# Kernel optimization log

Hardware: AMD Instinct MI355X
Metric: run time of the kernel (lower is better)

Reference implementation:

```python
import jax, jax.numpy as jnp
import numpy as np

D_SVG, N_TYPE, N_PAR = 256, 10, 12          # deep-svg latent, animation types, animation params
PADDING_VALUE = -1.0
W_SVG, W_TYPE, W_PAR = 10.0, 0.1, 1.0       # weight_deep_svg, weight_type, weight_parameters

# ANIMATION_PARAMETER_INDICES as a dense boolean lookup: type t -> which params it uses
_pm = np.zeros((N_TYPE, N_PAR), dtype=bool)
for _t in range(N_TYPE):
    for _k in (_t % N_PAR, (_t + 1) % N_PAR, (_t + 2) % N_PAR):
        _pm[_t, _k] = True
PARAM_MASK = jnp.asarray(_pm)


def setup_inputs() -> dict:
    B, S = 256, 512
    F = D_SVG + N_TYPE + N_PAR
    key = jax.random.key(0)
    k1, k2, k3, k4, k5 = jax.random.split(key, 5)
    x = jax.random.normal(k1, (B, S, F), dtype=jnp.float32)
    cls = jax.random.randint(k2, (B, S), 0, N_TYPE)
    t_type = jax.nn.one_hot(cls, N_TYPE, dtype=jnp.float32)
    t_svg = jax.random.normal(k3, (B, S, D_SVG), dtype=jnp.float32)
    t_par = jax.random.normal(k4, (B, S, N_PAR), dtype=jnp.float32)
    target = jnp.concatenate([t_svg, t_type, t_par], axis=-1)
    # suffix-contiguous padding (matches the `break` semantics of the torch loop)
    lengths = jax.random.randint(k5, (B,), S // 2, S + 1)
    mask = jnp.arange(S)[None, :] >= lengths[:, None]            # True = padded
    target = jnp.where(mask[..., None], PADDING_VALUE, target)
    return {"input": x, "target": target, "target_padding_mask": mask}


def reference(input, target, target_padding_mask):
    # input[expanded_mask] = -100
    x = jnp.where(target_padding_mask[..., None], -100.0, input)
    in_svg, in_type, in_par = jnp.split(x, [D_SVG, D_SVG + N_TYPE], axis=-1)
    tg_svg, tg_type, tg_par = jnp.split(target, [D_SVG, D_SVG + N_TYPE], axis=-1)

    valid = tg_type[..., 0] != PADDING_VALUE                      # [B,S] non-padded rows
    t_idx = jnp.argmax(tg_type, axis=-1)                          # [B,S] animation type

    # vectorized replacement of the double for-loop: copy target params at the
    # type-dependent ANIMATION_PARAMETER_INDICES into input params
    pmask = PARAM_MASK[t_idx] & valid[..., None]                  # [B,S,N_PAR]
    in_par = jnp.where(pmask, tg_par, in_par)

    # CrossEntropyLoss(ignore_index=-1) over flattened type logits
    logits = in_type.reshape(-1, N_TYPE)
    labels = t_idx.reshape(-1)
    v = valid.reshape(-1).astype(logits.dtype)
    logp = jax.nn.log_softmax(logits, axis=-1)
    nll = -jnp.take_along_axis(logp, labels[:, None], axis=1)[:, 0]
    loss_type = jnp.sum(nll * v) / jnp.maximum(jnp.sum(v), 1.0)

    # plain MSE (mean over ALL elements, padding included, as in the original)
    loss_svg = jnp.mean((in_svg - tg_svg) ** 2)
    loss_par = jnp.mean((in_par - tg_par) ** 2)

    return W_SVG * loss_svg + W_TYPE * loss_type + W_PAR * loss_par
```

## Files before the change

### kernel.cpp

```cpp
#include <hip/hip_runtime.h>
#include <hip/hip_bf16.h>
#include <math.h>

#define D_SVG 256
#define N_TYPE 10
#define N_PAR 12
#define F_TOT (D_SVG + N_TYPE + N_PAR)
#define ROWS_PER_BLOCK 32
#define THREADS 256
#define N4_PER_BLOCK (ROWS_PER_BLOCK * F_TOT / 4)
#define FULL_ITERS (N4_PER_BLOCK / THREADS)
#define TAIL (N4_PER_BLOCK - FULL_ITERS * THREADS)

#define PAD_SVG_BLOCK (9801.0f * D_SVG * ROWS_PER_BLOCK)
#define PAD_PAR_BLOCK (9801.0f * N_PAR * ROWS_PER_BLOCK)


__global__ __launch_bounds__(THREADS) void loss_main(const float* __restrict__ input,
                                                     const float* __restrict__ target,
                                                     float4* __restrict__ part,
                                                     int nrows) {
    __shared__ unsigned smeta[ROWS_PER_BLOCK];
    __shared__ unsigned long long sballot;
    __shared__ float sred[4][4];

    const int tid = threadIdx.x;
    const long row0 = (long)blockIdx.x * ROWS_PER_BLOCK;

    float nll_acc = 0.0f;
    float cnt_acc = 0.0f;

    if (tid < ROWS_PER_BLOCK) {
        unsigned meta = 0u;
        long r = row0 + tid;
        long b2 = (r * F_TOT + D_SVG) >> 1;
        const float2* __restrict__ tg2 = (const float2*)target;
        const float2* __restrict__ in2 = (const float2*)input;
        float2 t01 = tg2[b2];
        if (t01.x != -1.0f) {
            float tg[N_TYPE], l[N_TYPE];
            tg[0] = t01.x; tg[1] = t01.y;
            #pragma unroll
            for (int j = 1; j < 5; ++j) { float2 v = tg2[b2 + j]; tg[2*j] = v.x; tg[2*j+1] = v.y; }
            #pragma unroll
            for (int j = 0; j < 5; ++j) { float2 v = in2[b2 + j]; l[2*j] = v.x; l[2*j+1] = v.y; }
            int ti = 0; float best = tg[0];
            #pragma unroll
            for (int j = 1; j < N_TYPE; ++j) { if (tg[j] > best) { best = tg[j]; ti = j; } }
            float m = l[0];
            #pragma unroll
            for (int j = 1; j < N_TYPE; ++j) m = fmaxf(m, l[j]);
            float s = 0.0f;
            #pragma unroll
            for (int j = 0; j < N_TYPE; ++j) s += __expf(l[j] - m);
            nll_acc = __logf(s) + m - l[ti];
            cnt_acc = 1.0f;
            meta = 0x80000000u | (7u << ti);
        }
        smeta[tid] = meta;
        unsigned long long bal = __ballot(meta != 0u);
        if (tid == 0) sballot = bal;
    }
    __syncthreads();

    if (sballot == 0ull) {
        if (tid == 0) part[blockIdx.x] = make_float4(PAD_SVG_BLOCK, PAD_PAR_BLOCK, 0.0f, 0.0f);
        return;
    }

    float svg_acc = 0.0f, par_acc = 0.0f;
    const float4* __restrict__ in4p = (const float4*)(input + row0 * F_TOT);
    const float4* __restrict__ tg4p = (const float4*)(target + row0 * F_TOT);

    float4 iv[FULL_ITERS], tv[FULL_ITERS];
    #pragma unroll
    for (int u = 0; u < FULL_ITERS; ++u) iv[u] = in4p[tid + u * THREADS];
    #pragma unroll
    for (int u = 0; u < FULL_ITERS; ++u) tv[u] = tg4p[tid + u * THREADS];

    auto accum = [&](int idx, float4 ivv, float4 tvv) {
        unsigned e0 = (unsigned)idx * 4u;
        unsigned ra = e0 / (unsigned)F_TOT;
        unsigned rb = (e0 + 2u) / (unsigned)F_TOT;
        unsigned fa = e0 - ra * (unsigned)F_TOT;
        unsigned fb = (e0 + 2u) - rb * (unsigned)F_TOT;
        unsigned ma = smeta[ra];
        unsigned mb = smeta[rb];
        float xs[4] = {ivv.x, ivv.y, ivv.z, ivv.w};
        float ts[4] = {tvv.x, tvv.y, tvv.z, tvv.w};
        #pragma unroll
        for (int j = 0; j < 4; ++j) {
            unsigned meta = (j < 2) ? ma : mb;
            unsigned feat = ((j < 2) ? fa : fb) + (unsigned)(j & 1);
            float x = (meta & 0x80000000u) ? xs[j] : -100.0f;
            float d = x - ts[j];
            float sq = d * d;
            if (feat < D_SVG) {
                svg_acc += sq;
            } else if (feat >= D_SVG + N_TYPE) {
                unsigned k = feat - (D_SVG + N_TYPE);
                par_acc += ((meta >> k) & 1u) ? 0.0f : sq;
            }
        }
    };

    #pragma unroll
    for (int u = 0; u < FULL_ITERS; ++u) accum(tid + u * THREADS, iv[u], tv[u]);
    if (tid < TAIL) {
        int idx = FULL_ITERS * THREADS + tid;
        accum(idx, in4p[idx], tg4p[idx]);
    }

    float vals[4] = {svg_acc, par_acc, nll_acc, cnt_acc};
    #pragma unroll
    for (int v = 0; v < 4; ++v) {
        float x = vals[v];
        #pragma unroll
        for (int off = 32; off > 0; off >>= 1) x += __shfl_down(x, off, 64);
        vals[v] = x;
    }
    const int wave = tid >> 6;
    const int lane = tid & 63;
    if (lane == 0) {
        #pragma unroll
        for (int v = 0; v < 4; ++v) sred[wave][v] = vals[v];
    }
    __syncthreads();
    if (tid == 0) {
        float s0 = sred[0][0] + sred[1][0] + sred[2][0] + sred[3][0];
        float s1 = sred[0][1] + sred[1][1] + sred[2][1] + sred[3][1];
        float s2 = sred[0][2] + sred[1][2] + sred[2][2] + sred[3][2];
        float s3 = sred[0][3] + sred[1][3] + sred[2][3] + sred[3][3];
        part[blockIdx.x] = make_float4(s0, s1, s2, s3);
    }
}

__global__ __launch_bounds__(256) void loss_reduce(const float4* __restrict__ part,
                                                   float* __restrict__ out, int nblocks,
                                                   double inv_svg_n, double inv_par_n) {
    __shared__ double sred[4][4];
    const int tid = threadIdx.x;
    double sv = 0.0, pa = 0.0, nl = 0.0, ct = 0.0;
    for (int i = tid; i < nblocks; i += 256) {
        float4 v = part[i];
        sv += v.x; pa += v.y; nl += v.z; ct += v.w;
    }
    double vals[4] = {sv, pa, nl, ct};
    #pragma unroll
    for (int v = 0; v < 4; ++v) {
        double x = vals[v];
        #pragma unroll
        for (int off = 32; off > 0; off >>= 1) x += __shfl_down(x, off, 64);
        vals[v] = x;
    }
    const int wave = tid >> 6;
    const int lane = tid & 63;
    if (lane == 0) {
        #pragma unroll
        for (int v = 0; v < 4; ++v) sred[wave][v] = vals[v];
    }
    __syncthreads();
    if (tid == 0) {
        double svg = sred[0][0] + sred[1][0] + sred[2][0] + sred[3][0];
        double par = sred[0][1] + sred[1][1] + sred[2][1] + sred[3][1];
        double nll = sred[0][2] + sred[1][2] + sred[2][2] + sred[3][2];
        double cnt = sred[0][3] + sred[1][3] + sred[2][3] + sred[3][3];
        double loss = 10.0 * svg * inv_svg_n
                    + 0.1 * nll / fmax(cnt, 1.0)
                    + 1.0 * par * inv_par_n;
        out[0] = (float)loss;
    }
}

extern "C" void kernel_launch(void* const* d_in, const int* in_sizes, int n_in,
                              void* d_out, int out_size, void* d_ws, size_t ws_size,
                              hipStream_t stream) {
    const float* input  = (const float*)d_in[0];
    const float* target = (const float*)d_in[1];
    float*  out  = (float*)d_out;
    float4* part = (float4*)d_ws;

    const int nrows = in_sizes[0] / F_TOT;
    const int blocks = nrows / ROWS_PER_BLOCK;

    loss_main<<<blocks, THREADS, 0, stream>>>(input, target, part, nrows);
    loss_reduce<<<1, 256, 0, stream>>>(part, out, blocks,
                                       1.0 / ((double)nrows * D_SVG),
                                       1.0 / ((double)nrows * N_PAR));
}
```

Baseline: 316.9 us.

## Split per-row metadata into separate kernel with validity bitmap and analytic padding

Moves the per-row type/CE computation into a separate kernel that also builds a 32-bit validity bitmap per 32-row block. The bulk MSE kernel then reads only the bitmap instead of doing the serialized per-block metadata phase and a barrier. Padded-row contributions are added analytically in the final reduction. The parameter-copy effect is handled by subtracting the three copied squared differences as a correction term. The cost is an extra kernel launch and a second read of the type/param columns, while the bulk kernel loses its prologue latency.

```diff
diff --git a/kernel.cpp b/kernel.cpp
--- a/kernel.cpp
+++ b/kernel.cpp
@@ -12,162 +12,183 @@
 #define FULL_ITERS (N4_PER_BLOCK / THREADS)
 #define TAIL (N4_PER_BLOCK - FULL_ITERS * THREADS)
 
-#define PAD_SVG_BLOCK (9801.0f * D_SVG * ROWS_PER_BLOCK)
-#define PAD_PAR_BLOCK (9801.0f * N_PAR * ROWS_PER_BLOCK)
-
-
-__global__ __launch_bounds__(THREADS) void loss_main(const float* __restrict__ input,
-                                                     const float* __restrict__ target,
-                                                     float4* __restrict__ part,
-                                                     int nrows) {
-    __shared__ unsigned smeta[ROWS_PER_BLOCK];
-    __shared__ unsigned long long sballot;
-    __shared__ float sred[4][4];
-
+
+__global__ __launch_bounds__(THREADS) void meta_kernel(const float* __restrict__ input,
+                                                       const float* __restrict__ target,
+                                                       float4* __restrict__ part_a,
+                                                       unsigned* __restrict__ bitmap) {
+    __shared__ float sred[4][3];
     const int tid = threadIdx.x;
-    const long row0 = (long)blockIdx.x * ROWS_PER_BLOCK;
-
-    float nll_acc = 0.0f;
-    float cnt_acc = 0.0f;
-
-    if (tid < ROWS_PER_BLOCK) {
-        unsigned meta = 0u;
-        long r = row0 + tid;
-        long b2 = (r * F_TOT + D_SVG) >> 1;
-        const float2* __restrict__ tg2 = (const float2*)target;
-        const float2* __restrict__ in2 = (const float2*)input;
-        float2 t01 = tg2[b2];
-        if (t01.x != -1.0f) {
-            float tg[N_TYPE], l[N_TYPE];
-            tg[0] = t01.x; tg[1] = t01.y;
-            #pragma unroll
-            for (int j = 1; j < 5; ++j) { float2 v = tg2[b2 + j]; tg[2*j] = v.x; tg[2*j+1] = v.y; }
-            #pragma unroll
-            for (int j = 0; j < 5; ++j) { float2 v = in2[b2 + j]; l[2*j] = v.x; l[2*j+1] = v.y; }
-            int ti = 0; float best = tg[0];
-            #pragma unroll
-            for (int j = 1; j < N_TYPE; ++j) { if (tg[j] > best) { best = tg[j]; ti = j; } }
-            float m = l[0];
-            #pragma unroll
-            for (int j = 1; j < N_TYPE; ++j) m = fmaxf(m, l[j]);
-            float s = 0.0f;
-            #pragma unroll
-            for (int j = 0; j < N_TYPE; ++j) s += __expf(l[j] - m);
-            nll_acc = __logf(s) + m - l[ti];
-            cnt_acc = 1.0f;
-            meta = 0x80000000u | (7u << ti);
-        }
-        smeta[tid] = meta;
-        unsigned long long bal = __ballot(meta != 0u);
-        if (tid == 0) sballot = bal;
-    }
-    __syncthreads();
-
-    if (sballot == 0ull) {
-        if (tid == 0) part[blockIdx.x] = make_float4(PAD_SVG_BLOCK, PAD_PAR_BLOCK, 0.0f, 0.0f);
-        return;
-    }
-
-    float svg_acc = 0.0f, par_acc = 0.0f;
-    const float4* __restrict__ in4p = (const float4*)(input + row0 * F_TOT);
-    const float4* __restrict__ tg4p = (const float4*)(target + row0 * F_TOT);
-
-    float4 iv[FULL_ITERS], tv[FULL_ITERS];
-    #pragma unroll
-    for (int u = 0; u < FULL_ITERS; ++u) iv[u] = in4p[tid + u * THREADS];
-    #pragma unroll
-    for (int u = 0; u < FULL_ITERS; ++u) tv[u] = tg4p[tid + u * THREADS];
-
-    auto accum = [&](int idx, float4 ivv, float4 tvv) {
-        unsigned e0 = (unsigned)idx * 4u;
-        unsigned ra = e0 / (unsigned)F_TOT;
-        unsigned rb = (e0 + 2u) / (unsigned)F_TOT;
-        unsigned fa = e0 - ra * (unsigned)F_TOT;
-        unsigned fb = (e0 + 2u) - rb * (unsigned)F_TOT;
-        unsigned ma = smeta[ra];
-        unsigned mb = smeta[rb];
-        float xs[4] = {ivv.x, ivv.y, ivv.z, ivv.w};
-        float ts[4] = {tvv.x, tvv.y, tvv.z, tvv.w};
-        #pragma unroll
-        for (int j = 0; j < 4; ++j) {
-            unsigned meta = (j < 2) ? ma : mb;
-            unsigned feat = ((j < 2) ? fa : fb) + (unsigned)(j & 1);
-            float x = (meta & 0x80000000u) ? xs[j] : -100.0f;
-            float d = x - ts[j];
-            float sq = d * d;
-            if (feat < D_SVG) {
-                svg_acc += sq;
-            } else if (feat >= D_SVG + N_TYPE) {
-                unsigned k = feat - (D_SVG + N_TYPE);
-                par_acc += ((meta >> k) & 1u) ? 0.0f : sq;
-            }
-        }
-    };
-
-    #pragma unroll
-    for (int u = 0; u < FULL_ITERS; ++u) accum(tid + u * THREADS, iv[u], tv[u]);
-    if (tid < TAIL) {
-        int idx = FULL_ITERS * THREADS + tid;
-        accum(idx, in4p[idx], tg4p[idx]);
-    }
-
-    float vals[4] = {svg_acc, par_acc, nll_acc, cnt_acc};
-    #pragma unroll
-    for (int v = 0; v < 4; ++v) {
+    const int r = blockIdx.x * THREADS + tid;
+
+    const float2* __restrict__ tg2 = (const float2*)target;
+    const float2* __restrict__ in2 = (const float2*)input;
+    const long b2 = ((long)r * F_TOT + D_SVG) >> 1;
+
+    float nll = 0.0f, cnt = 0.0f, corr = 0.0f;
+    float2 t01 = tg2[b2];
+    const bool valid = (t01.x != -1.0f);
+    if (valid) {
+        float tt[N_TYPE], l[N_TYPE];
+        tt[0] = t01.x; tt[1] = t01.y;
+        #pragma unroll
+        for (int j = 1; j < 5; ++j) { float2 v = tg2[b2 + j]; tt[2*j] = v.x; tt[2*j+1] = v.y; }
+        #pragma unroll
+        for (int j = 0; j < 5; ++j) { float2 v = in2[b2 + j]; l[2*j] = v.x; l[2*j+1] = v.y; }
+        int ti = 0; float best = tt[0];
+        #pragma unroll
+        for (int j = 1; j < N_TYPE; ++j) { if (tt[j] > best) { best = tt[j]; ti = j; } }
+        float m = l[0];
+        #pragma unroll
+        for (int j = 1; j < N_TYPE; ++j) m = fmaxf(m, l[j]);
+        float s = 0.0f;
+        #pragma unroll
+        for (int j = 0; j < N_TYPE; ++j) s += __expf(l[j] - m);
+        nll = __logf(s) + m - l[ti];
+        cnt = 1.0f;
+        const long p = (long)r * F_TOT + (D_SVG + N_TYPE) + ti;
+        float d0 = input[p]     - target[p];
+        float d1 = input[p + 1] - target[p + 1];
+        float d2 = input[p + 2] - target[p + 2];
+        corr = d0 * d0 + d1 * d1 + d2 * d2;
+    }
+
+    unsigned long long bal = __ballot(valid);
+    const int lane = tid & 63, wv = tid >> 6;
+    if (lane == 0)  bitmap[blockIdx.x * 8 + wv * 2]     = (unsigned)bal;
+    if (lane == 32) bitmap[blockIdx.x * 8 + wv * 2 + 1] = (unsigned)(bal >> 32);
+
+    float vals[3] = {nll, cnt, corr};
+    #pragma unroll
+    for (int v = 0; v < 3; ++v) {
         float x = vals[v];
         #pragma unroll
         for (int off = 32; off > 0; off >>= 1) x += __shfl_down(x, off, 64);
         vals[v] = x;
     }
-    const int wave = tid >> 6;
-    const int lane = tid & 63;
     if (lane == 0) {
         #pragma unroll
-        for (int v = 0; v < 4; ++v) sred[wave][v] = vals[v];
+        for (int v = 0; v < 3; ++v) sred[wv][v] = vals[v];
     }
     __syncthreads();
     if (tid == 0) {
         float s0 = sred[0][0] + sred[1][0] + sred[2][0] + sred[3][0];
         float s1 = sred[0][1] + sred[1][1] + sred[2][1] + sred[3][1];
         float s2 = sred[0][2] + sred[1][2] + sred[2][2] + sred[3][2];
-        float s3 = sred[0][3] + sred[1][3] + sred[2][3] + sred[3][3];
-        part[blockIdx.x] = make_float4(s0, s1, s2, s3);
-    }
-}
-
-__global__ __launch_bounds__(256) void loss_reduce(const float4* __restrict__ part,
-                                                   float* __restrict__ out, int nblocks,
-                                                   double inv_svg_n, double inv_par_n) {
-    __shared__ double sred[4][4];
+        part_a[blockIdx.x] = make_float4(s0, s1, s2, 0.0f);
+    }
+}
+
+__global__ __launch_bounds__(THREADS) void bulk_kernel(const float* __restrict__ input,
+                                                       const float* __restrict__ target,
+                                                       const unsigned* __restrict__ bitmap,
+                                                       float4* __restrict__ part_b) {
+    __shared__ float sred[4][2];
     const int tid = threadIdx.x;
-    double sv = 0.0, pa = 0.0, nl = 0.0, ct = 0.0;
-    for (int i = tid; i < nblocks; i += 256) {
-        float4 v = part[i];
-        sv += v.x; pa += v.y; nl += v.z; ct += v.w;
-    }
-    double vals[4] = {sv, pa, nl, ct};
-    #pragma unroll
-    for (int v = 0; v < 4; ++v) {
-        double x = vals[v];
+    const unsigned bits = bitmap[blockIdx.x];
+
+    if (bits == 0u) {
+        if (tid == 0) part_b[blockIdx.x] = make_float4(0.f, 0.f, 0.f, 0.f);
+        return;
+    }
+
+    const long row0 = (long)blockIdx.x * ROWS_PER_BLOCK;
+    const float4* __restrict__ in4p = (const float4*)(input + row0 * F_TOT);
+    const float4* __restrict__ tg4p = (const float4*)(target + row0 * F_TOT);
+
+    float svg_acc = 0.0f, par_acc = 0.0f;
+
+    auto accum = [&](unsigned idx, float4 ivv, float4 tvv) {
+        unsigned e0 = idx * 4u;
+        unsigned ra = e0 / (unsigned)F_TOT;
+        unsigned rb = (e0 + 2u) / (unsigned)F_TOT;
+        unsigned fa = e0 - ra * (unsigned)F_TOT;
+        unsigned fb = (e0 + 2u) - rb * (unsigned)F_TOT;
+        unsigned vA = (bits >> ra) & 1u;
+        unsigned vB = (bits >> rb) & 1u;
+        float xs[4] = {ivv.x, ivv.y, ivv.z, ivv.w};
+        float ts[4] = {tvv.x, tvv.y, tvv.z, tvv.w};
+        #pragma unroll
+        for (int j = 0; j < 4; ++j) {
+            unsigned v    = (j < 2) ? vA : vB;
+            unsigned feat = ((j < 2) ? fa : fb) + (unsigned)(j & 1);
+            float d = xs[j] - ts[j];
+            float sq = d * d;
+            svg_acc += (v && feat < D_SVG) ? sq : 0.0f;
+            par_acc += (v && feat >= D_SVG + N_TYPE) ? sq : 0.0f;
+        }
+    };
+
+    float4 iv[FULL_ITERS], tv[FULL_ITERS];
+    #pragma unroll
+    for (int u = 0; u < FULL_ITERS; ++u) iv[u] = in4p[tid + u * THREADS];
+    #pragma unroll
+    for (int u = 0; u < FULL_ITERS; ++u) tv[u] = tg4p[tid + u * THREADS];
+    #pragma unroll
+    for (int u = 0; u < FULL_ITERS; ++u) accum(tid + u * THREADS, iv[u], tv[u]);
+    if (tid < TAIL) {
+        unsigned idx = FULL_ITERS * THREADS + tid;
+        accum(idx, in4p[idx], tg4p[idx]);
+    }
+
+    float vals[2] = {svg_acc, par_acc};
+    #pragma unroll
+    for (int v = 0; v < 2; ++v) {
+        float x = vals[v];
         #pragma unroll
         for (int off = 32; off > 0; off >>= 1) x += __shfl_down(x, off, 64);
         vals[v] = x;
     }
-    const int wave = tid >> 6;
-    const int lane = tid & 63;
-    if (lane == 0) {
-        #pragma unroll
-        for (int v = 0; v < 4; ++v) sred[wave][v] = vals[v];
-    }
+    const int wave = tid >> 6, lane = tid & 63;
+    if (lane == 0) { sred[wave][0] = vals[0]; sred[wave][1] = vals[1]; }
     __syncthreads();
     if (tid == 0) {
-        double svg = sred[0][0] + sred[1][0] + sred[2][0] + sred[3][0];
-        double par = sred[0][1] + sred[1][1] + sred[2][1] + sred[3][1];
-        double nll = sred[0][2] + sred[1][2] + sred[2][2] + sred[3][2];
-        double cnt = sred[0][3] + sred[1][3] + sred[2][3] + sred[3][3];
-        double loss = 10.0 * svg * inv_svg_n
-                    + 0.1 * nll / fmax(cnt, 1.0)
-                    + 1.0 * par * inv_par_n;
+        float s0 = sred[0][0] + sred[1][0] + sred[2][0] + sred[3][0];
+        float s1 = sred[0][1] + sred[1][1] + sred[2][1] + sred[3][1];
+        part_b[blockIdx.x] = make_float4(s0, s1, 0.0f, 0.0f);
+    }
+}
+
+__global__ __launch_bounds__(256) void loss_final(const float4* __restrict__ part_b,
+                                                  const float4* __restrict__ part_a,
+                                                  float* __restrict__ out,
+                                                  int nb, int na, int nrows) {
+    __shared__ double sred[4][5];
+    const int tid = threadIdx.x;
+    double svg = 0.0, par = 0.0, nll = 0.0, cnt = 0.0, corr = 0.0;
+    for (int i = tid; i < nb; i += 256) {
+        float4 v = part_b[i];
+        svg += v.x; par += v.y;
+    }
+    for (int i = tid; i < na; i += 256) {
+        float4 v = part_a[i];
+        nll += v.x; cnt += v.y; corr += v.z;
+    }
+    double vals[5] = {svg, par, nll, cnt, corr};
+    #pragma unroll
+    for (int v = 0; v < 5; ++v) {
+        double x = vals[v];
+        #pragma unroll
+        for (int off = 32; off > 0; off >>= 1) x += __shfl_down(x, off, 64);
+        vals[v] = x;
+    }
+    const int wave = tid >> 6, lane = tid & 63;
+    if (lane == 0) {
+        #pragma unroll
+        for (int v = 0; v < 5; ++v) sred[wave][v] = vals[v];
+    }
+    __syncthreads();
+    if (tid == 0) {
+        double S[5];
+        #pragma unroll
+        for (int v = 0; v < 5; ++v)
+            S[v] = sred[0][v] + sred[1][v] + sred[2][v] + sred[3][v];
+        double npad = (double)nrows - S[3];
+        double svg_t = S[0] + 9801.0 * D_SVG * npad;
+        double par_t = S[1] - S[4] + 9801.0 * N_PAR * npad;
+        double loss = 10.0 * svg_t / ((double)nrows * D_SVG)
+                    + 0.1  * S[2] / fmax(S[3], 1.0)
+                    + 1.0  * par_t / ((double)nrows * N_PAR);
         out[0] = (float)loss;
     }
 }
@@ -177,14 +198,17 @@
                               hipStream_t stream) {
     const float* input  = (const float*)d_in[0];
     const float* target = (const float*)d_in[1];
-    float*  out  = (float*)d_out;
-    float4* part = (float4*)d_ws;
-
-    const int nrows = in_sizes[0] / F_TOT;
-    const int blocks = nrows / ROWS_PER_BLOCK;
-
-    loss_main<<<blocks, THREADS, 0, stream>>>(input, target, part, nrows);
-    loss_reduce<<<1, 256, 0, stream>>>(part, out, blocks,
-                                       1.0 / ((double)nrows * D_SVG),
-                                       1.0 / ((double)nrows * N_PAR));
-}
+    float* out = (float*)d_out;
+
+    const int nrows  = in_sizes[0] / F_TOT;
+    const int blk_b  = nrows / ROWS_PER_BLOCK;
+    const int blk_a  = nrows / THREADS;
+
+    float4*   part_b = (float4*)d_ws;
+    float4*   part_a = (float4*)((char*)d_ws + (size_t)blk_b * sizeof(float4));
+    unsigned* bitmap = (unsigned*)((char*)part_a + (size_t)blk_a * sizeof(float4));
+
+    meta_kernel<<<blk_a, THREADS, 0, stream>>>(input, target, part_a, bitmap);
+    bulk_kernel<<<blk_b, THREADS, 0, stream>>>(input, target, bitmap, part_b);
+    loss_final<<<1, 256, 0, stream>>>(part_b, part_a, out, blk_b, blk_a, nrows);
+}
```

Result: faster. 299.9 us (-5.4%).
